# Kernel optimization log

Measured on AMD Instinct MI355X. Metric: run time of the kernel, lower is better.

Reference implementation:

```python
import jax, jax.numpy as jnp
import numpy as np

N, E, IN, H, OUT, K = 50000, 800000, 128, 128, 40, 10
ALPHA, EPS, AH = 0.1, 1e-5, 64


def setup_inputs() -> dict:
    key = jax.random.key(0)
    ks = jax.random.split(key, 32)
    rn = lambda k, s, sc=0.05: jax.random.normal(k, s, jnp.float32) * sc
    return dict(
        x=jax.random.normal(ks[0], (N, IN), jnp.float32),
        edge_index=jax.random.randint(ks[1], (2, E), 0, N, jnp.int64),
        edge_weight=jax.random.uniform(ks[2], (E,), jnp.float32),
        lin1_w=rn(ks[3], (H, IN)), lin1_b=rn(ks[4], (H,)),
        bn1_g=jnp.ones((H,), jnp.float32), bn1_b=jnp.zeros((H,), jnp.float32),
        bn1_m=rn(ks[5], (H,)), bn1_v=jax.random.uniform(ks[6], (H,), jnp.float32, 0.5, 1.5),
        lin2_w=rn(ks[7], (H, H)), lin2_b=rn(ks[8], (H,)),
        bn2_g=jnp.ones((H,), jnp.float32), bn2_b=jnp.zeros((H,), jnp.float32),
        bn2_m=rn(ks[9], (H,)), bn2_v=jax.random.uniform(ks[10], (H,), jnp.float32, 0.5, 1.5),
        att1_w=rn(ks[11], (AH, 2 * H)), att1_b=rn(ks[12], (AH,)),
        att2_w=rn(ks[13], (K + 1, AH)), att2_b=rn(ks[14], (K + 1,)),
        head1_w=rn(ks[15], (H // 2, H)), head1_b=rn(ks[16], (H // 2,)),
        bn3_g=jnp.ones((H // 2,), jnp.float32), bn3_b=jnp.zeros((H // 2,), jnp.float32),
        bn3_m=rn(ks[17], (H // 2,)), bn3_v=jax.random.uniform(ks[18], (H // 2,), jnp.float32, 0.5, 1.5),
        head2_w=rn(ks[19], (OUT, H // 2)), head2_b=rn(ks[20], (OUT,)),
    )


def _bn(x, g, b, m, v):
    # eval-mode BatchNorm1d with running stats
    return (x - m) * jax.lax.rsqrt(v + EPS) * g + b


def reference(x, edge_index, edge_weight,
              lin1_w, lin1_b, bn1_g, bn1_b, bn1_m, bn1_v,
              lin2_w, lin2_b, bn2_g, bn2_b, bn2_m, bn2_v,
              att1_w, att1_b, att2_w, att2_b,
              head1_w, head1_b, bn3_g, bn3_b, bn3_m, bn3_v,
              head2_w, head2_b):
    row, col = edge_index[0], edge_index[1]

    # dense stem (dropout is identity in eval mode)
    h = jax.nn.relu(_bn(x @ lin1_w.T + lin1_b, bn1_g, bn1_b, bn1_m, bn1_v))
    identity = h
    h = jax.nn.relu(_bn(h @ lin2_w.T + lin2_b, bn2_g, bn2_b, bn2_m, bn2_v)) + identity
    base = h  # h0 for APPNP

    # edge normalization (loop-invariant): w_e / clamp(sum_w(row), 1)
    wsum = jnp.clip(jax.ops.segment_sum(edge_weight, row, num_segments=N), 1.0)
    enorm = edge_weight / wsum[row]  # [E]

    xs = [h]
    for _ in range(K):  # fixed K iterations of gather -> scatter-add
        agg = jax.ops.segment_sum(h[row] * enorm[:, None], col, num_segments=N)
        h = (1.0 - ALPHA) * agg + ALPHA * base
        xs.append(h)

    stacked = jnp.stack(xs, axis=-1)                    # [N, H, K+1]
    ctx = jnp.concatenate([xs[0], xs[-1]], axis=-1)     # [N, 2H]
    a = jax.nn.gelu(ctx @ att1_w.T + att1_b, approximate=False) @ att2_w.T + att2_b
    w = jax.nn.softmax(a, axis=-1)[:, None, :]          # [N, 1, K+1]
    fused = (stacked * w).sum(axis=-1)                  # [N, H]

    z = jax.nn.relu(_bn(fused @ head1_w.T + head1_b, bn3_g, bn3_b, bn3_m, bn3_v))
    return z @ head2_w.T + head2_b
```

## Files before the change

kernel.cpp:

```cpp
#include <hip/hip_runtime.h>
#include <hip/hip_fp16.h>
#include <math.h>

#define NN 50000
#define EE 800000
#define HH 128
#define KIT 10
#define NHF (NN * HH)
#define PST 16

typedef _Float16 half8 __attribute__((ext_vector_type(8)));
typedef float floatx4 __attribute__((ext_vector_type(4)));

__device__ __forceinline__ float gelu_exact(float x) {
  return 0.5f * x * (1.f + erff(x * 0.70710678118654752f));
}

__device__ __forceinline__ float4 ld4(const float* p) { return *(const float4*)p; }
__device__ __forceinline__ float4 ld4(const __half* p) {
  const __half2* q = (const __half2*)p;
  float2 lo = __half22float2(q[0]);
  float2 hi = __half22float2(q[1]);
  return make_float4(lo.x, lo.y, hi.x, hi.y);
}
__device__ __forceinline__ void st1(float* p, float v) { *p = v; }
__device__ __forceinline__ void st1(__half* p, float v) { *p = __float2half_rn(v); }

__global__ __launch_bounds__(256) void zero_kernel(float* __restrict__ wsum_p,
                                                   int* __restrict__ deg_p, int n) {
  int i = blockIdx.x * 256 + threadIdx.x;
  if (i < n) { wsum_p[i] = 0.f; deg_p[i] = 0; }
}

__global__ __launch_bounds__(256) void edge_stats_kernel(const int* __restrict__ ei,
                                                         const float* __restrict__ ew,
                                                         float* __restrict__ wsum_p,
                                                         int* __restrict__ deg_p,
                                                         int* __restrict__ rank, int e_cnt) {
  int e = blockIdx.x * 256 + threadIdx.x;
  if (e >= e_cnt) return;
  atomicAdd(&wsum_p[(size_t)ei[e] * PST], ew[e]);
  rank[e] = atomicAdd(&deg_p[(size_t)ei[EE + e] * PST], 1);
}

__global__ __launch_bounds__(256) void scan1_kernel(const int* __restrict__ deg_p,
                                                    int* __restrict__ bsum, int n) {
  __shared__ int red[256];
  int i = blockIdx.x * 256 + threadIdx.x;
  red[threadIdx.x] = (i < n) ? deg_p[(size_t)i * PST] : 0;
  __syncthreads();
  for (int off = 128; off > 0; off >>= 1) {
    if (threadIdx.x < off) red[threadIdx.x] += red[threadIdx.x + off];
    __syncthreads();
  }
  if (threadIdx.x == 0) bsum[blockIdx.x] = red[0];
}

__global__ __launch_bounds__(256) void scan2_kernel(const int* __restrict__ bsum,
                                                    int* __restrict__ boff,
                                                    int* __restrict__ row_start, int nb, int n) {
  __shared__ int buf[256];
  int tid = threadIdx.x;
  int v = (tid < nb) ? bsum[tid] : 0;
  buf[tid] = v;
  __syncthreads();
  for (int off = 1; off < 256; off <<= 1) {
    int t = (tid >= off) ? buf[tid - off] : 0;
    __syncthreads();
    buf[tid] += t;
    __syncthreads();
  }
  if (tid < nb) boff[tid] = buf[tid] - v;
  if (tid == 255) row_start[n] = buf[255];
}

__global__ __launch_bounds__(256) void scan3_kernel(const int* __restrict__ deg_p,
                                                    const int* __restrict__ boff,
                                                    int* __restrict__ row_start, int n) {
  __shared__ int buf[256];
  int tid = threadIdx.x;
  int i = blockIdx.x * 256 + tid;
  int v = (i < n) ? deg_p[(size_t)i * PST] : 0;
  buf[tid] = v;
  __syncthreads();
  for (int off = 1; off < 256; off <<= 1) {
    int t = (tid >= off) ? buf[tid - off] : 0;
    __syncthreads();
    buf[tid] += t;
    __syncthreads();
  }
  if (i < n) row_start[i] = boff[blockIdx.x] + buf[tid] - v;
}

__global__ __launch_bounds__(256) void csr_fill_kernel(const int* __restrict__ ei,
                                                       const float* __restrict__ ew,
                                                       const float* __restrict__ wsum_p,
                                                       const int* __restrict__ row_start,
                                                       const int* __restrict__ rank,
                                                       int2* __restrict__ csr, int e_cnt) {
  int e = blockIdx.x * 256 + threadIdx.x;
  if (e >= e_cnt) return;
  int r = ei[e], c = ei[EE + e];
  float ws = wsum_p[(size_t)r * PST];
  ws = ws < 1.f ? 1.f : ws;
  float v = 0.9f * ew[e] / ws;
  int pos = row_start[c] + rank[e];
  csr[pos] = make_int2(r, __float_as_int(v));
}

__global__ __launch_bounds__(256) void prop_kernel(const __half* __restrict__ h_cur,
                                                   const __half* __restrict__ base,
                                                   const int* __restrict__ row_start,
                                                   const long* __restrict__ csr,
                                                   __half* __restrict__ h_next) {
  int node = __builtin_amdgcn_readfirstlane((int)blockIdx.x * 4 + (int)(threadIdx.x >> 6));
  if (node >= NN) return;
  int lane = threadIdx.x & 63;
  const __half2* hc = (const __half2*)h_cur;
  float2 b = __half22float2(((const __half2*)base)[(size_t)node * 64 + lane]);
  float ax = 0.1f * b.x, ay = 0.1f * b.y;
  float bx = 0.f, by = 0.f;
  int s = row_start[node], e = row_start[node + 1];
  int nfull = (e - s) >> 3;
  int i = s;
  if (nfull > 0) {
    long cur[8];
#pragma unroll
    for (int j = 0; j < 8; ++j) cur[j] = csr[i + j];
    i += 8;
    for (int bidx = 1; bidx < nfull; ++bidx) {
      long nxt[8];
#pragma unroll
      for (int j = 0; j < 8; ++j) nxt[j] = csr[i + j];
      i += 8;
      float2 g[8];
#pragma unroll
      for (int j = 0; j < 8; ++j) g[j] = __half22float2(hc[(size_t)(int)cur[j] * 64 + lane]);
#pragma unroll
      for (int j = 0; j < 8; ++j) {
        float v = __int_as_float((int)(cur[j] >> 32));
        if (j & 1) { bx = fmaf(v, g[j].x, bx); by = fmaf(v, g[j].y, by); }
        else       { ax = fmaf(v, g[j].x, ax); ay = fmaf(v, g[j].y, ay); }
      }
#pragma unroll
      for (int j = 0; j < 8; ++j) cur[j] = nxt[j];
    }
    float2 g[8];
#pragma unroll
    for (int j = 0; j < 8; ++j) g[j] = __half22float2(hc[(size_t)(int)cur[j] * 64 + lane]);
#pragma unroll
    for (int j = 0; j < 8; ++j) {
      float v = __int_as_float((int)(cur[j] >> 32));
      if (j & 1) { bx = fmaf(v, g[j].x, bx); by = fmaf(v, g[j].y, by); }
      else       { ax = fmaf(v, g[j].x, ax); ay = fmaf(v, g[j].y, ay); }
    }
  }
  for (; i < e; ++i) {
    long c0 = csr[i];
    float2 g0 = __half22float2(hc[(size_t)(int)c0 * 64 + lane]);
    float v = __int_as_float((int)(c0 >> 32));
    ax = fmaf(v, g0.x, ax); ay = fmaf(v, g0.y, ay);
  }
  ((__half2*)h_next)[(size_t)node * 64 + lane] =
      __float22half2_rn(make_float2(ax + bx, ay + by));
}

template <int K, int KA, int JP, int JR, int ACT, bool RESID, typename IT, typename OT>
__global__ __launch_bounds__(256) void mfma_dense(
    const IT* __restrict__ Xa, const IT* __restrict__ Xb,
    const float* __restrict__ W, const float* __restrict__ lb,
    const float* __restrict__ bg, const float* __restrict__ bb,
    const float* __restrict__ bm, const float* __restrict__ bv,
    const OT* __restrict__ resid, OT* __restrict__ out) {
  constexpr int KC = (K > 128) ? 128 : K;
  static_assert(K % KC == 0 && KC % 32 == 0 && JP % 16 == 0, "");
  constexpr int JT = JP / 16;
  __shared__ _Float16 xL[128][KC + 8];
  __shared__ _Float16 wL[JP][KC + 8];
  const int tid = threadIdx.x;
  const int wv = tid >> 6, lane = tid & 63;
  const int q = lane >> 4, m = lane & 15;
  const int r0 = blockIdx.x * 128;

  floatx4 acc[2][JT];
#pragma unroll
  for (int rt = 0; rt < 2; ++rt)
#pragma unroll
    for (int jt = 0; jt < JT; ++jt) acc[rt][jt] = (floatx4)(0.f);

  for (int kc = 0; kc < K; kc += KC) {
    __syncthreads();
    for (int idx = tid; idx < 128 * (KC / 4); idx += 256) {
      int r = idx / (KC / 4);
      int c4 = (idx % (KC / 4)) * 4;
      int row = r0 + r;
      int col = kc + c4;
      float4 v = make_float4(0.f, 0.f, 0.f, 0.f);
      if (row < NN) {
        if (col < KA) v = ld4(&Xa[(size_t)row * KA + col]);
        else          v = ld4(&Xb[(size_t)row * (K - KA) + (col - KA)]);
      }
      xL[r][c4 + 0] = (_Float16)v.x; xL[r][c4 + 1] = (_Float16)v.y;
      xL[r][c4 + 2] = (_Float16)v.z; xL[r][c4 + 3] = (_Float16)v.w;
    }
    for (int idx = tid; idx < JP * (KC / 4); idx += 256) {
      int j = idx / (KC / 4);
      int c4 = (idx % (KC / 4)) * 4;
      float4 v = make_float4(0.f, 0.f, 0.f, 0.f);
      if (j < JR) v = *(const float4*)&W[(size_t)j * K + kc + c4];
      wL[j][c4 + 0] = (_Float16)v.x; wL[j][c4 + 1] = (_Float16)v.y;
      wL[j][c4 + 2] = (_Float16)v.z; wL[j][c4 + 3] = (_Float16)v.w;
    }
    __syncthreads();
#pragma unroll
    for (int ks = 0; ks < KC; ks += 32) {
      half8 a0 = *(const half8*)&xL[wv * 32 + m][ks + q * 8];
      half8 a1 = *(const half8*)&xL[wv * 32 + 16 + m][ks + q * 8];
#pragma unroll
      for (int jt = 0; jt < JT; ++jt) {
        half8 b = *(const half8*)&wL[jt * 16 + m][ks + q * 8];
        acc[0][jt] = __builtin_amdgcn_mfma_f32_16x16x32_f16(a0, b, acc[0][jt], 0, 0, 0);
        acc[1][jt] = __builtin_amdgcn_mfma_f32_16x16x32_f16(a1, b, acc[1][jt], 0, 0, 0);
      }
    }
  }
#pragma unroll
  for (int jt = 0; jt < JT; ++jt) {
    int j = jt * 16 + m;
    if (j >= JR) continue;
    float sc = 0.f, sh = 0.f;
    if (ACT == 1) {
      sc = bg[j] * rsqrtf(bv[j] + 1e-5f);
      sh = (lb[j] - bm[j]) * sc + bb[j];
    } else {
      sh = lb[j];
    }
#pragma unroll
    for (int rt = 0; rt < 2; ++rt) {
#pragma unroll
      for (int reg = 0; reg < 4; ++reg) {
        int row = r0 + wv * 32 + rt * 16 + q * 4 + reg;
        if (row >= NN) continue;
        float a = acc[rt][jt][reg];
        float y;
        if (ACT == 0)      y = a + sh;
        else if (ACT == 1) y = fmaxf(fmaf(a, sc, sh), 0.f);
        else               y = gelu_exact(a + sh);
        if (RESID) y += (float)resid[(size_t)row * JR + j];
        st1(&out[(size_t)row * JR + j], y);
      }
    }
  }
}

__global__ __launch_bounds__(64) void att2_softmax_kernel(const __half* __restrict__ g,
                                                          const float* __restrict__ W2,
                                                          const float* __restrict__ b2,
                                                          float* __restrict__ attw, int n_rows) {
  __shared__ float gl[64][65];
  int r0 = blockIdx.x * 64;
  for (int idx = threadIdx.x; idx < 64 * 16; idx += 64) {
    int r = idx >> 4, c4 = (idx & 15) * 4;
    float4 v = make_float4(0.f, 0.f, 0.f, 0.f);
    if (r0 + r < n_rows) v = ld4(&g[(size_t)(r0 + r) * 64 + c4]);
    gl[r][c4] = v.x; gl[r][c4 + 1] = v.y; gl[r][c4 + 2] = v.z; gl[r][c4 + 3] = v.w;
  }
  __syncthreads();
  int r = threadIdx.x;
  int n = r0 + r;
  if (n >= n_rows) return;
  float a[KIT + 1];
#pragma unroll
  for (int j = 0; j < KIT + 1; ++j) {
    float acc = b2[j];
#pragma unroll
    for (int k = 0; k < 64; ++k) acc = fmaf(gl[r][k], W2[j * 64 + k], acc);
    a[j] = acc;
  }
  float mx = a[0];
#pragma unroll
  for (int j = 1; j < KIT + 1; ++j) mx = fmaxf(mx, a[j]);
  float s = 0.f;
#pragma unroll
  for (int j = 0; j < KIT + 1; ++j) { a[j] = expf(a[j] - mx); s += a[j]; }
  float inv = 1.f / s;
#pragma unroll
  for (int j = 0; j < KIT + 1; ++j) attw[n * 16 + j] = a[j] * inv;
}

__global__ __launch_bounds__(256) void fused_gather_kernel(const __half* __restrict__ XS,
                                                           const float* __restrict__ attw,
                                                           __half* __restrict__ fused) {
  int node = __builtin_amdgcn_readfirstlane((int)blockIdx.x * 4 + (int)(threadIdx.x >> 6));
  if (node >= NN) return;
  int lane = threadIdx.x & 63;
  float ax = 0.f, ay = 0.f;
#pragma unroll
  for (int k = 0; k <= KIT; ++k) {
    float wk = attw[node * 16 + k];
    float2 v = __half22float2(((const __half2*)(XS + (size_t)k * NHF))[(size_t)node * 64 + lane]);
    ax = fmaf(wk, v.x, ax);
    ay = fmaf(wk, v.y, ay);
  }
  ((__half2*)fused)[(size_t)node * 64 + lane] = __float22half2_rn(make_float2(ax, ay));
}

__global__ __launch_bounds__(256) void fused_accum_kernel(const __half* __restrict__ h,
                                                          const float* __restrict__ attw,
                                                          float* __restrict__ fused, int k) {
  int node = __builtin_amdgcn_readfirstlane((int)blockIdx.x * 4 + (int)(threadIdx.x >> 6));
  if (node >= NN) return;
  int lane = threadIdx.x & 63;
  float wk = attw[node * 16 + k];
  float2 v = __half22float2(((const __half2*)h)[(size_t)node * 64 + lane]);
  float2 o;
  if (k == 0) {
    o = make_float2(wk * v.x, wk * v.y);
  } else {
    float2 f = ((const float2*)fused)[(size_t)node * 64 + lane];
    o = make_float2(fmaf(wk, v.x, f.x), fmaf(wk, v.y, f.y));
  }
  ((float2*)fused)[(size_t)node * 64 + lane] = o;
}

extern "C" void kernel_launch(void* const* d_in, const int* in_sizes, int n_in,
                              void* d_out, int out_size, void* d_ws, size_t ws_size,
                              hipStream_t stream) {
  (void)in_sizes; (void)n_in; (void)out_size;
  const float* x      = (const float*)d_in[0];
  const int*   ei     = (const int*)d_in[1];
  const float* ew     = (const float*)d_in[2];
  const float* lin1_w = (const float*)d_in[3];
  const float* lin1_b = (const float*)d_in[4];
  const float* bn1_g  = (const float*)d_in[5];
  const float* bn1_b  = (const float*)d_in[6];
  const float* bn1_m  = (const float*)d_in[7];
  const float* bn1_v  = (const float*)d_in[8];
  const float* lin2_w = (const float*)d_in[9];
  const float* lin2_b = (const float*)d_in[10];
  const float* bn2_g  = (const float*)d_in[11];
  const float* bn2_b  = (const float*)d_in[12];
  const float* bn2_m  = (const float*)d_in[13];
  const float* bn2_v  = (const float*)d_in[14];
  const float* att1_w = (const float*)d_in[15];
  const float* att1_b = (const float*)d_in[16];
  const float* att2_w = (const float*)d_in[17];
  const float* att2_b = (const float*)d_in[18];
  const float* head1_w= (const float*)d_in[19];
  const float* head1_b= (const float*)d_in[20];
  const float* bn3_g  = (const float*)d_in[21];
  const float* bn3_b  = (const float*)d_in[22];
  const float* bn3_m  = (const float*)d_in[23];
  const float* bn3_v  = (const float*)d_in[24];
  const float* head2_w= (const float*)d_in[25];
  const float* head2_b= (const float*)d_in[26];
  float* out = (float*)d_out;

  char* p = (char*)d_ws;
  auto alloc = [&](size_t bytes) -> void* {
    void* r = (void*)p;
    p += (bytes + 255) & ~(size_t)255;
    return r;
  };
  int*   row_start= (int*)alloc((size_t)(NN + 1) * 4);
  int*   bsum     = (int*)alloc((size_t)256 * 4);
  int*   boff     = (int*)alloc((size_t)256 * 4);
  long*  csr      = (long*)alloc((size_t)EE * 8);
  __half* gbuf    = (__half*)alloc((size_t)NN * 64 * 2);
  float* attw     = (float*)alloc((size_t)NN * 16 * 4);
  __half* h1      = (__half*)alloc((size_t)NHF * 2);
  __half* fusedH  = (__half*)alloc((size_t)NHF * 2);
  __half* zbuf    = (__half*)alloc((size_t)NN * 64 * 2);
  size_t common = (size_t)(p - (char*)d_ws);
  size_t stored_need = common + (size_t)(KIT + 1) * NHF * 2 + 4096;
  bool stored = ws_size >= stored_need;

  __half* XS = nullptr;
  float* wsum_p; int* deg_p; int* rank;
  if (stored) {
    XS = (__half*)alloc((size_t)(KIT + 1) * NHF * 2);
    char* ovl = (char*)(XS + (size_t)KIT * NHF);
    wsum_p = (float*)ovl;
    deg_p  = (int*)(ovl + (size_t)NN * PST * 4);
    rank   = (int*)(ovl + 2 * (size_t)NN * PST * 4);
  } else {
    wsum_p = (float*)alloc((size_t)NN * PST * 4);
    deg_p  = (int*)alloc((size_t)NN * PST * 4);
    rank   = (int*)alloc((size_t)EE * 4);
  }

  const int GE  = (EE + 255) / 256;
  const int GN  = (NN + 255) / 256;
  const int GN0 = (NN * PST + 255) / 256;
  const int GM  = (NN + 127) / 128;
  const int GP  = (NN + 3) / 4;
  const int GA  = (NN + 63) / 64;

  zero_kernel<<<GN0, 256, 0, stream>>>(wsum_p, deg_p, NN * PST);
  edge_stats_kernel<<<GE, 256, 0, stream>>>(ei, ew, wsum_p, deg_p, rank, EE);
  scan1_kernel<<<GN, 256, 0, stream>>>(deg_p, bsum, NN);
  scan2_kernel<<<1, 256, 0, stream>>>(bsum, boff, row_start, GN, NN);
  scan3_kernel<<<GN, 256, 0, stream>>>(deg_p, boff, row_start, NN);
  csr_fill_kernel<<<GE, 256, 0, stream>>>(ei, ew, wsum_p, row_start, rank, (int2*)csr, EE);

  if (stored) {
    mfma_dense<128, 128, 128, 128, 1, false, float, __half><<<GM, 256, 0, stream>>>(
        x, (const float*)nullptr, lin1_w, lin1_b, bn1_g, bn1_b, bn1_m, bn1_v, nullptr, h1);
    mfma_dense<128, 128, 128, 128, 1, true, __half, __half><<<GM, 256, 0, stream>>>(
        h1, (const __half*)nullptr, lin2_w, lin2_b, bn2_g, bn2_b, bn2_m, bn2_v, h1, XS);
    for (int k = 0; k < KIT; ++k) {
      prop_kernel<<<GP, 256, 0, stream>>>(XS + (size_t)k * NHF, XS, row_start,
                                          csr, XS + (size_t)(k + 1) * NHF);
    }
    mfma_dense<256, 128, 64, 64, 2, false, __half, __half><<<GM, 256, 0, stream>>>(
        XS, XS + (size_t)KIT * NHF, att1_w, att1_b, nullptr, nullptr, nullptr, nullptr,
        nullptr, gbuf);
    att2_softmax_kernel<<<GA, 64, 0, stream>>>(gbuf, att2_w, att2_b, attw, NN);
    fused_gather_kernel<<<GP, 256, 0, stream>>>(XS, attw, fusedH);
    mfma_dense<128, 128, 64, 64, 1, false, __half, __half><<<GM, 256, 0, stream>>>(
        fusedH, (const __half*)nullptr, head1_w, head1_b, bn3_g, bn3_b, bn3_m, bn3_v,
        nullptr, zbuf);
  } else {
    float*  fusedF = (float*)alloc((size_t)NHF * 4);
    __half* base   = (__half*)alloc((size_t)NHF * 2);
    __half* hA     = (__half*)alloc((size_t)NHF * 2);
    __half* hB     = (__half*)alloc((size_t)NHF * 2);
    mfma_dense<128, 128, 128, 128, 1, false, float, __half><<<GM, 256, 0, stream>>>(
        x, (const float*)nullptr, lin1_w, lin1_b, bn1_g, bn1_b, bn1_m, bn1_v, nullptr, h1);
    mfma_dense<128, 128, 128, 128, 1, true, __half, __half><<<GM, 256, 0, stream>>>(
        h1, (const __half*)nullptr, lin2_w, lin2_b, bn2_g, bn2_b, bn2_m, bn2_v, h1, base);
    const __half* cur = base;
    for (int k = 1; k <= KIT; ++k) {
      __half* nxt = (k & 1) ? hA : hB;
      prop_kernel<<<GP, 256, 0, stream>>>(cur, base, row_start, csr, nxt);
      cur = nxt;
    }
    mfma_dense<256, 128, 64, 64, 2, false, __half, __half><<<GM, 256, 0, stream>>>(
        base, cur, att1_w, att1_b, nullptr, nullptr, nullptr, nullptr, nullptr, gbuf);
    att2_softmax_kernel<<<GA, 64, 0, stream>>>(gbuf, att2_w, att2_b, attw, NN);
    fused_accum_kernel<<<GP, 256, 0, stream>>>(base, attw, fusedF, 0);
    cur = base;
    for (int k = 1; k <= KIT; ++k) {
      __half* nxt = (k & 1) ? hA : hB;
      prop_kernel<<<GP, 256, 0, stream>>>(cur, base, row_start, csr, nxt);
      fused_accum_kernel<<<GP, 256, 0, stream>>>(nxt, attw, fusedF, k);
      cur = nxt;
    }
    mfma_dense<128, 128, 64, 64, 1, false, float, __half><<<GM, 256, 0, stream>>>(
        fusedF, (const float*)nullptr, head1_w, head1_b, bn3_g, bn3_b, bn3_m, bn3_v,
        nullptr, zbuf);
  }

  mfma_dense<64, 64, 48, 40, 0, false, __half, float><<<GM, 256, 0, stream>>>(
      zbuf, (const __half*)nullptr, head2_w, head2_b, nullptr, nullptr, nullptr, nullptr,
      nullptr, out);
}
```

Before: 660.6 us.

## Build CSR via per-chunk shared-memory histograms instead of global atomics

Replaces the global-atomic degree and weight-sum pass (padded counters plus a zeroing kernel) with a 2D grid of blocks. Each block builds shared-memory histograms for one edge chunk and one node range, then writes per-chunk partial counts. A reduce kernel turns these into exclusive per-chunk offsets, totals and block sums, and the CSR fill combines the row start, the chunk offset and the local rank. This removes contended global atomics and the strided padded memory, at the cost of each block scanning its whole edge chunk once per node range and extra partial arrays of CC×NN entries.

```diff
diff --git a/kernel.cpp b/kernel.cpp
--- a/kernel.cpp
+++ b/kernel.cpp
@@ -7,7 +7,10 @@
 #define HH 128
 #define KIT 10
 #define NHF (NN * HH)
-#define PST 16
+#define RR 8
+#define CC 64
+#define NR (NN / RR)
+#define CH (EE / CC)
 
 typedef _Float16 half8 __attribute__((ext_vector_type(8)));
 typedef float floatx4 __attribute__((ext_vector_type(4)));
@@ -26,28 +29,52 @@
 __device__ __forceinline__ void st1(float* p, float v) { *p = v; }
 __device__ __forceinline__ void st1(__half* p, float v) { *p = __float2half_rn(v); }
 
-__global__ __launch_bounds__(256) void zero_kernel(float* __restrict__ wsum_p,
-                                                   int* __restrict__ deg_p, int n) {
-  int i = blockIdx.x * 256 + threadIdx.x;
-  if (i < n) { wsum_p[i] = 0.f; deg_p[i] = 0; }
-}
-
-__global__ __launch_bounds__(256) void edge_stats_kernel(const int* __restrict__ ei,
-                                                         const float* __restrict__ ew,
-                                                         float* __restrict__ wsum_p,
-                                                         int* __restrict__ deg_p,
-                                                         int* __restrict__ rank, int e_cnt) {
-  int e = blockIdx.x * 256 + threadIdx.x;
-  if (e >= e_cnt) return;
-  atomicAdd(&wsum_p[(size_t)ei[e] * PST], ew[e]);
-  rank[e] = atomicAdd(&deg_p[(size_t)ei[EE + e] * PST], 1);
-}
-
-__global__ __launch_bounds__(256) void scan1_kernel(const int* __restrict__ deg_p,
-                                                    int* __restrict__ bsum, int n) {
+__global__ __launch_bounds__(256) void hist_kernel(const int* __restrict__ ei,
+                                                   const float* __restrict__ ew,
+                                                   int* __restrict__ pdeg,
+                                                   float* __restrict__ pwsum,
+                                                   int* __restrict__ rank) {
+  __shared__ int hist[NR];
+  __shared__ float whist[NR];
+  const int c = blockIdx.x, r = blockIdx.y;
+  const int lo = r * NR;
+  for (int i = threadIdx.x; i < NR; i += 256) { hist[i] = 0; whist[i] = 0.f; }
+  __syncthreads();
+  const int e0 = c * CH;
+  for (int i = threadIdx.x; i < CH; i += 256) {
+    int e = e0 + i;
+    int src = ei[e], dst = ei[EE + e];
+    unsigned us = (unsigned)(src - lo), ud = (unsigned)(dst - lo);
+    if (us < NR) atomicAdd(&whist[us], ew[e]);
+    if (ud < NR) rank[e] = atomicAdd(&hist[ud], 1);
+  }
+  __syncthreads();
+  for (int i = threadIdx.x; i < NR; i += 256) {
+    pdeg [(size_t)c * NN + lo + i] = hist[i];
+    pwsum[(size_t)c * NN + lo + i] = whist[i];
+  }
+}
+
+__global__ __launch_bounds__(256) void reduce_kernel(int* __restrict__ pdeg,
+                                                     const float* __restrict__ pwsum,
+                                                     int* __restrict__ deg,
+                                                     float* __restrict__ wsum,
+                                                     int* __restrict__ bsum) {
+  int node = blockIdx.x * 256 + threadIdx.x;
+  int acc = 0; float wacc = 0.f;
+  if (node < NN) {
+    for (int c = 0; c < CC; ++c) {
+      size_t idx = (size_t)c * NN + node;
+      int t = pdeg[idx];
+      pdeg[idx] = acc;
+      acc += t;
+      wacc += pwsum[idx];
+    }
+    deg[node] = acc;
+    wsum[node] = wacc;
+  }
   __shared__ int red[256];
-  int i = blockIdx.x * 256 + threadIdx.x;
-  red[threadIdx.x] = (i < n) ? deg_p[(size_t)i * PST] : 0;
+  red[threadIdx.x] = (node < NN) ? acc : 0;
   __syncthreads();
   for (int off = 128; off > 0; off >>= 1) {
     if (threadIdx.x < off) red[threadIdx.x] += red[threadIdx.x + off];
@@ -74,13 +101,13 @@
   if (tid == 255) row_start[n] = buf[255];
 }
 
-__global__ __launch_bounds__(256) void scan3_kernel(const int* __restrict__ deg_p,
+__global__ __launch_bounds__(256) void scan3_kernel(const int* __restrict__ deg,
                                                     const int* __restrict__ boff,
                                                     int* __restrict__ row_start, int n) {
   __shared__ int buf[256];
   int tid = threadIdx.x;
   int i = blockIdx.x * 256 + tid;
-  int v = (i < n) ? deg_p[(size_t)i * PST] : 0;
+  int v = (i < n) ? deg[i] : 0;
   buf[tid] = v;
   __syncthreads();
   for (int off = 1; off < 256; off <<= 1) {
@@ -94,18 +121,20 @@
 
 __global__ __launch_bounds__(256) void csr_fill_kernel(const int* __restrict__ ei,
                                                        const float* __restrict__ ew,
-                                                       const float* __restrict__ wsum_p,
+                                                       const float* __restrict__ wsum,
                                                        const int* __restrict__ row_start,
+                                                       const int* __restrict__ pdeg_excl,
                                                        const int* __restrict__ rank,
                                                        int2* __restrict__ csr, int e_cnt) {
   int e = blockIdx.x * 256 + threadIdx.x;
   if (e >= e_cnt) return;
-  int r = ei[e], c = ei[EE + e];
-  float ws = wsum_p[(size_t)r * PST];
+  int c = e / CH;
+  int src = ei[e], dst = ei[EE + e];
+  float ws = wsum[src];
   ws = ws < 1.f ? 1.f : ws;
   float v = 0.9f * ew[e] / ws;
-  int pos = row_start[c] + rank[e];
-  csr[pos] = make_int2(r, __float_as_int(v));
+  int pos = row_start[dst] + pdeg_excl[(size_t)c * NN + dst] + rank[e];
+  csr[pos] = make_int2(src, __float_as_int(v));
 }
 
 __global__ __launch_bounds__(256) void prop_kernel(const __half* __restrict__ h_cur,
@@ -365,6 +394,8 @@
   int*   row_start= (int*)alloc((size_t)(NN + 1) * 4);
   int*   bsum     = (int*)alloc((size_t)256 * 4);
   int*   boff     = (int*)alloc((size_t)256 * 4);
+  int*   deg      = (int*)alloc((size_t)NN * 4);
+  float* wsum     = (float*)alloc((size_t)NN * 4);
   long*  csr      = (long*)alloc((size_t)EE * 8);
   __half* gbuf    = (__half*)alloc((size_t)NN * 64 * 2);
   float* attw     = (float*)alloc((size_t)NN * 16 * 4);
@@ -376,32 +407,31 @@
   bool stored = ws_size >= stored_need;
 
   __half* XS = nullptr;
-  float* wsum_p; int* deg_p; int* rank;
+  int* pdeg; float* pwsum; int* rank;
   if (stored) {
     XS = (__half*)alloc((size_t)(KIT + 1) * NHF * 2);
-    char* ovl = (char*)(XS + (size_t)KIT * NHF);
-    wsum_p = (float*)ovl;
-    deg_p  = (int*)(ovl + (size_t)NN * PST * 4);
-    rank   = (int*)(ovl + 2 * (size_t)NN * PST * 4);
+    char* ovl = (char*)(XS + (size_t)8 * NHF);
+    pdeg  = (int*)ovl;
+    pwsum = (float*)(ovl + (size_t)CC * NN * 4);
+    rank  = (int*)(ovl + 2 * (size_t)CC * NN * 4);
   } else {
-    wsum_p = (float*)alloc((size_t)NN * PST * 4);
-    deg_p  = (int*)alloc((size_t)NN * PST * 4);
-    rank   = (int*)alloc((size_t)EE * 4);
+    pdeg  = (int*)alloc((size_t)CC * NN * 4);
+    pwsum = (float*)alloc((size_t)CC * NN * 4);
+    rank  = (int*)alloc((size_t)EE * 4);
   }
 
   const int GE  = (EE + 255) / 256;
   const int GN  = (NN + 255) / 256;
-  const int GN0 = (NN * PST + 255) / 256;
   const int GM  = (NN + 127) / 128;
   const int GP  = (NN + 3) / 4;
   const int GA  = (NN + 63) / 64;
 
-  zero_kernel<<<GN0, 256, 0, stream>>>(wsum_p, deg_p, NN * PST);
-  edge_stats_kernel<<<GE, 256, 0, stream>>>(ei, ew, wsum_p, deg_p, rank, EE);
-  scan1_kernel<<<GN, 256, 0, stream>>>(deg_p, bsum, NN);
+  hist_kernel<<<dim3(CC, RR), 256, 0, stream>>>(ei, ew, pdeg, pwsum, rank);
+  reduce_kernel<<<GN, 256, 0, stream>>>(pdeg, pwsum, deg, wsum, bsum);
   scan2_kernel<<<1, 256, 0, stream>>>(bsum, boff, row_start, GN, NN);
-  scan3_kernel<<<GN, 256, 0, stream>>>(deg_p, boff, row_start, NN);
-  csr_fill_kernel<<<GE, 256, 0, stream>>>(ei, ew, wsum_p, row_start, rank, (int2*)csr, EE);
+  scan3_kernel<<<GN, 256, 0, stream>>>(deg, boff, row_start, NN);
+  csr_fill_kernel<<<GE, 256, 0, stream>>>(ei, ew, wsum, row_start, pdeg, rank,
+                                          (int2*)csr, EE);
 
   if (stored) {
     mfma_dense<128, 128, 128, 128, 1, false, float, __half><<<GM, 256, 0, stream>>>(
```

Result: faster. 628.8 us (-4.8%).
